# Performance work log

Hardware: AMD Instinct MI355X
Metric: run time of the kernel (lower is better)

Reference implementation:

```python
import jax, jax.numpy as jnp
import numpy as np

H = 128
NG, NS, NP = 50000, 20000, 30000
NUM_PC_FEATURES = 5
EPS = 1e-12


def seg_sum(x, idx, n):
    return jax.ops.segment_sum(x, idx, num_segments=n)


def seg_mean(x, idx, n):
    s = seg_sum(x, idx, n)
    cnt = seg_sum(jnp.ones((x.shape[0],), x.dtype), idx, n)
    return s / jnp.maximum(cnt, 1.0)[:, None]


def gcn_norm(row, col, n, add_self_loops):
    deg = seg_sum(jnp.ones(row.shape, jnp.float32), col, n)
    if add_self_loops:
        deg = deg + 1.0
    dinv = jnp.where(deg > 0, deg ** -0.5, 0.0)
    return dinv[row] * dinv[col], dinv


def tag_conv(x, row, col, n, Ws, b):
    # TAGConv: out = sum_k (A_hat^k x) W_k + b, symmetric norm, no self loops
    norm, _ = gcn_norm(row, col, n, False)
    out = x @ Ws[0]
    h = x
    for k in range(1, Ws.shape[0]):
        h = seg_sum(norm[:, None] * h[row], col, n)
        out = out + h @ Ws[k]
    return out + b


def rgcn_conv(x, row, col, etype, n, W, root, b):
    # RGCNConv: per-relation mean aggregation + root transform
    h = jnp.einsum('nc,rcd->rnd', x, W)  # [R, N, H]
    msg = h[etype, row]                  # [E, H]
    cnt = jnp.zeros((n, W.shape[0]), x.dtype).at[col, etype].add(1.0)
    w = 1.0 / jnp.maximum(cnt[col, etype], 1.0)
    return seg_sum(msg * w[:, None], col, n) + x @ root + b


def gcn_layer(x, row, col, n, W, b):
    # GCNConv: self loops + symmetric normalization
    xW = x @ W
    norm, dinv = gcn_norm(row, col, n, True)
    return seg_sum(norm[:, None] * xW[row], col, n) + (dinv ** 2)[:, None] * xW + b


def sage_conv(xs, xd, row, col, nd, lw, lb, rw):
    # SAGEConv with mean aggregation, root weight, L2 output normalization
    m = seg_mean(xs[row], col, nd)
    out = m @ lw + lb + xd @ rw
    nrm = jnp.maximum(jnp.linalg.norm(out, axis=-1, keepdims=True), EPS)
    return out / nrm


def setup_inputs() -> dict:
    key = jax.random.key(0)
    ks = iter(jax.random.split(key, 64))

    def nrm(shape):
        return jax.random.normal(next(ks), shape, jnp.float32) * 0.05

    def edges(ns, nd, e):
        return jnp.stack([jax.random.randint(next(ks), (e,), 0, ns, jnp.int32),
                          jax.random.randint(next(ks), (e,), 0, nd, jnp.int32)])

    return dict(
        game_x=nrm((NG, 7)),
        state_x=nrm((NS, 6)),
        pc_x=nrm((NP, NUM_PC_FEATURES)),
        edge_index_v_v=edges(NG, NG, 500000),
        edge_type_v_v=jax.random.randint(next(ks), (500000,), 0, 3, jnp.int32),
        edge_index_history_v_s=edges(NG, NS, 300000),
        edge_attr_history_v_s=nrm((300000, 2)),
        edge_index_in_v_s=edges(NG, NS, 300000),
        edge_index_s_s=edges(NS, NS, 200000),
        edge_index_pc_pc=edges(NP, NP, 300000),
        edge_index_pc_state=edges(NP, NS, 200000),
        edge_index_state_pc=edges(NS, NP, 100000),
        tag10_w=nrm((4, 7, H)), tag10_b=nrm((H,)),
        rgcn_w=nrm((3, H, H)), rgcn_root=nrm((H, H)), rgcn_b=nrm((H,)),
        gcn1_w=nrm((NUM_PC_FEATURES, H)), gcn1_b=nrm((H,)),
        gcn2_w=nrm((H, H)), gcn2_b=nrm((H,)),
        rg_key_w=nrm((6, H)), rg_key_b=nrm((H,)),
        rg_query_w=nrm((H, H)), rg_query_b=nrm((H,)),
        rg_value_w=nrm((H, H)), rg_value_b=nrm((H,)),
        rg_edge_w=nrm((2, H)), rg_skip_w=nrm((6, H)), rg_b=nrm((H,)),
        sage32_lw=nrm((H, H)), sage32_lb=nrm((H,)), sage32_rw=nrm((H, H)),
        sage4_lw=nrm((H, H)), sage4_lb=nrm((H,)), sage4_rw=nrm((H, H)),
        sage42_lw=nrm((H, H)), sage42_lb=nrm((H,)), sage42_rw=nrm((H, H)),
        pcs_lw=nrm((H, H)), pcs_lb=nrm((H,)), pcs_rw=nrm((H, H)),
        tag2_w=nrm((3, H, H)), tag2_b=nrm((H,)),
        sage5_lw=nrm((H, H)), sage5_lb=nrm((H,)), sage5_rw=nrm((H, H)),
        lin_w=nrm((H, 32)), lin_b=nrm((32,)),
        linl_w=nrm((32, 1)), linl_b=nrm((1,)),
    )


def reference(game_x, state_x, pc_x, edge_index_v_v, edge_type_v_v,
              edge_index_history_v_s, edge_attr_history_v_s, edge_index_in_v_s,
              edge_index_s_s, edge_index_pc_pc, edge_index_pc_state, edge_index_state_pc,
              tag10_w, tag10_b, rgcn_w, rgcn_root, rgcn_b,
              gcn1_w, gcn1_b, gcn2_w, gcn2_b,
              rg_key_w, rg_key_b, rg_query_w, rg_query_b, rg_value_w, rg_value_b,
              rg_edge_w, rg_skip_w, rg_b,
              sage32_lw, sage32_lb, sage32_rw,
              sage4_lw, sage4_lb, sage4_rw,
              sage42_lw, sage42_lb, sage42_rw,
              pcs_lw, pcs_lb, pcs_rw,
              tag2_w, tag2_b,
              sage5_lw, sage5_lb, sage5_rw,
              lin_w, lin_b, linl_w, linl_b):
    relu = jax.nn.relu
    rvv, cvv = edge_index_v_v[0], edge_index_v_v[1]
    g = relu(tag_conv(game_x, rvv, cvv, NG, tag10_w, tag10_b))
    g = relu(rgcn_conv(g, rvv, cvv, edge_type_v_v, NG, rgcn_w, rgcn_root, rgcn_b))
    rp, cp = edge_index_pc_pc[0], edge_index_pc_pc[1]
    p = relu(gcn_layer(pc_x, rp, cp, NP, gcn1_w, gcn1_b))
    p = relu(gcn_layer(p, rp, cp, NP, gcn2_w, gcn2_b))
    rh, ch = edge_index_history_v_s[0], edge_index_history_v_s[1]
    # ResGatedGraphConv((game, state), H, edge_dim=2)
    kk = state_x @ rg_key_w + rg_key_b
    q = g @ rg_query_w + rg_query_b
    v = g @ rg_value_w + rg_value_b
    e = edge_attr_history_v_s @ rg_edge_w
    eta = jax.nn.sigmoid(kk[ch] + q[rh] + e)
    s = relu(seg_sum(eta * v[rh], ch, NS) + state_x @ rg_skip_w + rg_b)
    s = relu(sage_conv(g, s, rh, ch, NS, sage32_lw, sage32_lb, sage32_rw))
    ri, ci = edge_index_in_v_s[0], edge_index_in_v_s[1]
    s = relu(sage_conv(g, s, ri, ci, NS, sage4_lw, sage4_lb, sage4_rw))
    s = relu(sage_conv(g, s, ri, ci, NS, sage42_lw, sage42_lb, sage42_rw))
    rps, cps = edge_index_pc_state[0], edge_index_pc_state[1]
    s = relu(sage_conv(p, s, rps, cps, NS, pcs_lw, pcs_lb, pcs_rw))
    rs, cs = edge_index_s_s[0], edge_index_s_s[1]
    s = relu(tag_conv(s, rs, cs, NS, tag2_w, tag2_b))
    s = relu(sage_conv(s, s, rs, cs, NS, sage5_lw, sage5_lb, sage5_rw))
    s = relu(s @ lin_w + lin_b)
    return jax.nn.log_softmax(s @ linl_w + linl_b, axis=0)
```

## Files before the change

### kernel.cpp

```cpp
#include <hip/hip_runtime.h>
#include <cstdint>

#define H 128
static const int NG = 50000, NS = 20000, NP = 30000;

#define TG_RELU 2
#define TG_NORM 4
#define TG_OUTBF16 8

#define CSR_CHUNK 8192

typedef __attribute__((ext_vector_type(8))) short bf16x8;
typedef __attribute__((ext_vector_type(4))) float f32x4;
typedef __attribute__((ext_vector_type(2))) float v2f;

static inline int nblk(long long n) { return (int)((n + 255) / 256); }

__device__ inline unsigned short f2b(float f) {
  unsigned int u = __float_as_uint(f);
  u += 0x7FFFu + ((u >> 16) & 1u);
  return (unsigned short)(u >> 16);
}
__device__ inline float b2f(unsigned short u) {
  return __uint_as_float(((unsigned int)u) << 16);
}
__device__ inline float2 bfp2(unsigned int u) {
  return make_float2(__uint_as_float(u << 16), __uint_as_float(u & 0xFFFF0000u));
}
__device__ inline unsigned int f2bfp(float x, float y) {
  return ((unsigned int)f2b(y) << 16) | (unsigned int)f2b(x);
}
__device__ inline float2 f8p2(unsigned short u) {
  v2f r = __builtin_amdgcn_cvt_pk_f32_fp8((int)(unsigned int)u, false);
  return make_float2(r.x, r.y);
}
__device__ inline unsigned char f2f8(float x) {
  int r = __builtin_amdgcn_cvt_pk_fp8_f32(x, 0.f, 0, false);
  return (unsigned char)(r & 0xFF);
}

struct Seg6 {
  const int* col[6];
  const int* row[6];
  const int* et0;
  int nodeoff[7];
  int edgeoff[7];
  int mode[6];
  float addself[6];
  int hasdinv[6];
};

__global__ __launch_bounds__(256) void k_hist(Seg6 sg, int EE, int* __restrict__ table) {
  __shared__ int h[512];
  int tid = threadIdx.x, blk = blockIdx.x;
  h[tid] = 0; h[tid + 256] = 0;
  __syncthreads();
  int e0 = blk * CSR_CHUNK, e1 = min(EE, e0 + CSR_CHUNK);
  for (int e = e0 + tid; e < e1; e += 256) {
    int gi = 0;
    while (e >= sg.edgeoff[gi + 1]) gi++;
    int le = e - sg.edgeoff[gi];
    int gn = sg.nodeoff[gi] + sg.col[gi][le];
    atomicAdd(&h[gn >> 9], 1);
  }
  __syncthreads();
  table[blk * 512 + tid] = h[tid];
  table[blk * 512 + tid + 256] = h[tid + 256];
}

__global__ void k_scanT(int* __restrict__ table, int nblkA, int* __restrict__ coarseOff) {
  int b = threadIdx.x;
  int s = 0;
  for (int k = 0; k < nblkA; k++) s += table[k * 512 + b];
  __shared__ int cs[512];
  cs[b] = s;
  __syncthreads();
  for (int off = 1; off < 512; off <<= 1) {
    int v = cs[b];
    int u = (b >= off) ? cs[b - off] : 0;
    __syncthreads();
    cs[b] = v + u;
    __syncthreads();
  }
  int excl = (b > 0) ? cs[b - 1] : 0;
  coarseOff[b] = excl;
  if (b == 511) coarseOff[512] = cs[511];
  int run = excl;
  for (int k = 0; k < nblkA; k++) {
    int t = table[k * 512 + b];
    table[k * 512 + b] = run;
    run += t;
  }
}

__global__ __launch_bounds__(256) void k_scatterA(Seg6 sg, int EE, const int* __restrict__ table,
                                                  uint2* __restrict__ tmp) {
  __shared__ int cur[512];
  int tid = threadIdx.x, blk = blockIdx.x;
  cur[tid] = table[blk * 512 + tid];
  cur[tid + 256] = table[blk * 512 + tid + 256];
  __syncthreads();
  int e0 = blk * CSR_CHUNK, e1 = min(EE, e0 + CSR_CHUNK);
  for (int e = e0 + tid; e < e1; e += 256) {
    int gi = 0;
    while (e >= sg.edgeoff[gi + 1]) gi++;
    int le = e - sg.edgeoff[gi];
    int gn = sg.nodeoff[gi] + sg.col[gi][le];
    int m = sg.mode[gi];
    int pay;
    if (m == 2) pay = le;
    else {
      pay = sg.row[gi][le];
      if (m == 1) pay |= sg.et0[le] << 16;
    }
    int pos = atomicAdd(&cur[gn >> 9], 1);
    tmp[pos] = make_uint2((unsigned)gn, (unsigned)pay);
  }
}

__global__ __launch_bounds__(256) void k_localCSR(const uint2* __restrict__ tmp,
                                                  const int* __restrict__ coarseOff,
                                                  Seg6 sg, int NN, int EE, int B,
                                                  int* __restrict__ rowptr,
                                                  int* __restrict__ eidx,
                                                  float* __restrict__ dinv) {
  int b = blockIdx.x, tid = threadIdx.x;
  int base = b * 512;
  int nNodes = min(512, NN - base);
  int beg = coarseOff[b], end = coarseOff[b + 1];
  __shared__ int cnt[512];
  __shared__ int off[512];
  __shared__ int ps[256];
  cnt[tid] = 0; cnt[tid + 256] = 0;
  __syncthreads();
  for (int j = beg + tid; j < end; j += 256)
    atomicAdd(&cnt[tmp[j].x - base], 1);
  __syncthreads();
  int a = cnt[2 * tid], bb = cnt[2 * tid + 1];
  ps[tid] = a + bb;
  __syncthreads();
  for (int o = 1; o < 256; o <<= 1) {
    int v = ps[tid];
    int u = (tid >= o) ? ps[tid - o] : 0;
    __syncthreads();
    ps[tid] = v + u;
    __syncthreads();
  }
  int excl = (tid > 0) ? ps[tid - 1] : 0;
  off[2 * tid] = excl;
  off[2 * tid + 1] = excl + a;
  __syncthreads();
  for (int i = tid; i < nNodes; i += 256) {
    int gid = base + i;
    rowptr[gid] = beg + off[i];
    int gi = 0;
    while (gid >= sg.nodeoff[gi + 1]) gi++;
    if (sg.hasdinv[gi]) {
      float d = (float)cnt[i] + sg.addself[gi];
      dinv[gid] = (d > 0.f) ? rsqrtf(d) : 0.f;
    }
  }
  if (b == B - 1 && tid == 0) rowptr[NN] = EE;
  __syncthreads();
  for (int j = beg + tid; j < end; j += 256) {
    uint2 p = tmp[j];
    int pos = beg + atomicAdd(&off[p.x - base], 1);
    eidx[pos] = (int)p.y;
  }
}

struct PackD { const float* src; int Ksrc; int Kdst; };
struct Pack17 { PackD d[17]; int koff[18]; };

__global__ void k_pack(Pack17 p, unsigned short* __restrict__ Wt, int totalRows) {
  int t = blockIdx.x * blockDim.x + threadIdx.x;
  if (t >= totalRows * 128) return;
  int gk = t >> 7, n = t & 127;
  int w = 0;
  while (gk >= p.koff[w + 1]) w++;
  int k = gk - p.koff[w];
  float v = (k < p.d[w].Ksrc) ? p.d[w].src[(size_t)k * 128 + n] : 0.f;
  Wt[(size_t)p.koff[w] * 128 + (size_t)n * p.d[w].Kdst + k] = f2b(v);
}

__global__ __launch_bounds__(256) void k_gmean(const unsigned short* __restrict__ src,
                                               const int* __restrict__ eidx,
                                               const int* __restrict__ rowptr,
                                               unsigned short* __restrict__ out, int N) {
  int c = blockIdx.x * 4 + (threadIdx.x >> 6);
  if (c >= N) return;
  int lane = threadIdx.x & 63;
  int beg = rowptr[c], end = rowptr[c + 1];
  float2 A0 = {0.f, 0.f}, A1 = {0.f, 0.f}, A2 = {0.f, 0.f}, A3 = {0.f, 0.f};
  int j = beg;
  for (; j + 4 <= end; j += 4) {
    int e0 = eidx[j], e1 = eidx[j + 1], e2 = eidx[j + 2], e3 = eidx[j + 3];
    float2 v0 = bfp2(*(const unsigned int*)(src + (size_t)e0 * H + lane * 2));
    float2 v1 = bfp2(*(const unsigned int*)(src + (size_t)e1 * H + lane * 2));
    float2 v2 = bfp2(*(const unsigned int*)(src + (size_t)e2 * H + lane * 2));
    float2 v3 = bfp2(*(const unsigned int*)(src + (size_t)e3 * H + lane * 2));
    A0.x += v0.x; A0.y += v0.y;
    A1.x += v1.x; A1.y += v1.y;
    A2.x += v2.x; A2.y += v2.y;
    A3.x += v3.x; A3.y += v3.y;
  }
  for (; j < end; j++) {
    float2 v = bfp2(*(const unsigned int*)(src + (size_t)eidx[j] * H + lane * 2));
    A0.x += v.x; A0.y += v.y;
  }
  int cnt = end - beg;
  float s = 1.f / (float)(cnt > 0 ? cnt : 1);
  float ox = (A0.x + A1.x + A2.x + A3.x) * s;
  float oy = (A0.y + A1.y + A2.y + A3.y) * s;
  *(unsigned int*)(out + (size_t)c * H + lane * 2) = f2bfp(ox, oy);
}

__global__ __launch_bounds__(256) void k_gmean_f8(const unsigned char* __restrict__ src,
                                                  const int* __restrict__ eidx,
                                                  const int* __restrict__ rowptr,
                                                  unsigned short* __restrict__ out, int N) {
  int c = blockIdx.x * 4 + (threadIdx.x >> 6);
  if (c >= N) return;
  int lane = threadIdx.x & 63;
  int beg = rowptr[c], end = rowptr[c + 1];
  float2 A0 = {0.f, 0.f}, A1 = {0.f, 0.f}, A2 = {0.f, 0.f}, A3 = {0.f, 0.f};
  int j = beg;
  for (; j + 4 <= end; j += 4) {
    int e0 = eidx[j], e1 = eidx[j + 1], e2 = eidx[j + 2], e3 = eidx[j + 3];
    float2 v0 = f8p2(*(const unsigned short*)(src + (size_t)e0 * H + lane * 2));
    float2 v1 = f8p2(*(const unsigned short*)(src + (size_t)e1 * H + lane * 2));
    float2 v2 = f8p2(*(const unsigned short*)(src + (size_t)e2 * H + lane * 2));
    float2 v3 = f8p2(*(const unsigned short*)(src + (size_t)e3 * H + lane * 2));
    A0.x += v0.x; A0.y += v0.y;
    A1.x += v1.x; A1.y += v1.y;
    A2.x += v2.x; A2.y += v2.y;
    A3.x += v3.x; A3.y += v3.y;
  }
  for (; j < end; j++) {
    float2 v = f8p2(*(const unsigned short*)(src + (size_t)eidx[j] * H + lane * 2));
    A0.x += v.x; A0.y += v.y;
  }
  int cnt = end - beg;
  float s = 1.f / (float)(cnt > 0 ? cnt : 1);
  float ox = (A0.x + A1.x + A2.x + A3.x) * s;
  float oy = (A0.y + A1.y + A2.y + A3.y) * s;
  *(unsigned int*)(out + (size_t)c * H + lane * 2) = f2bfp(ox, oy);
}

__global__ __launch_bounds__(256) void k_grel3(const unsigned char* __restrict__ src,
                                               const int* __restrict__ eidx,
                                               const int* __restrict__ rowptr,
                                               unsigned short* __restrict__ G3, int N) {
  int c = blockIdx.x * 4 + (threadIdx.x >> 6);
  if (c >= N) return;
  int lane = threadIdx.x & 63;
  int beg = rowptr[c], end = rowptr[c + 1];
  float2 a0 = {0.f, 0.f}, a1 = {0.f, 0.f}, a2 = {0.f, 0.f};
  int c0 = 0, c1 = 0, c2 = 0;
  int j = beg;
  for (; j + 4 <= end; j += 4) {
    int p0 = eidx[j], p1 = eidx[j + 1], p2 = eidx[j + 2], p3 = eidx[j + 3];
    float2 w0 = f8p2(*(const unsigned short*)(src + (size_t)(p0 & 0xFFFF) * H + lane * 2));
    float2 w1 = f8p2(*(const unsigned short*)(src + (size_t)(p1 & 0xFFFF) * H + lane * 2));
    float2 w2 = f8p2(*(const unsigned short*)(src + (size_t)(p2 & 0xFFFF) * H + lane * 2));
    float2 w3 = f8p2(*(const unsigned short*)(src + (size_t)(p3 & 0xFFFF) * H + lane * 2));
    int r0 = p0 >> 16, r1 = p1 >> 16, r2 = p2 >> 16, r3 = p3 >> 16;
    if (r0 == 0) { a0.x += w0.x; a0.y += w0.y; c0++; }
    else if (r0 == 1) { a1.x += w0.x; a1.y += w0.y; c1++; }
    else { a2.x += w0.x; a2.y += w0.y; c2++; }
    if (r1 == 0) { a0.x += w1.x; a0.y += w1.y; c0++; }
    else if (r1 == 1) { a1.x += w1.x; a1.y += w1.y; c1++; }
    else { a2.x += w1.x; a2.y += w1.y; c2++; }
    if (r2 == 0) { a0.x += w2.x; a0.y += w2.y; c0++; }
    else if (r2 == 1) { a1.x += w2.x; a1.y += w2.y; c1++; }
    else { a2.x += w2.x; a2.y += w2.y; c2++; }
    if (r3 == 0) { a0.x += w3.x; a0.y += w3.y; c0++; }
    else if (r3 == 1) { a1.x += w3.x; a1.y += w3.y; c1++; }
    else { a2.x += w3.x; a2.y += w3.y; c2++; }
  }
  for (; j < end; j++) {
    int pk = eidx[j];
    int rel = pk >> 16;
    float2 v = f8p2(*(const unsigned short*)(src + (size_t)(pk & 0xFFFF) * H + lane * 2));
    if (rel == 0) { a0.x += v.x; a0.y += v.y; c0++; }
    else if (rel == 1) { a1.x += v.x; a1.y += v.y; c1++; }
    else { a2.x += v.x; a2.y += v.y; c2++; }
  }
  float s0 = 1.f / (float)(c0 > 0 ? c0 : 1);
  float s1 = 1.f / (float)(c1 > 0 ? c1 : 1);
  float s2 = 1.f / (float)(c2 > 0 ? c2 : 1);
  size_t base = (size_t)c * 384 + lane * 2;
  *(unsigned int*)(G3 + base) = f2bfp(a0.x * s0, a0.y * s0);
  *(unsigned int*)(G3 + base + 128) = f2bfp(a1.x * s1, a1.y * s1);
  *(unsigned int*)(G3 + base + 256) = f2bfp(a2.x * s2, a2.y * s2);
}

__global__ __launch_bounds__(256) void k_gnorm(const unsigned short* __restrict__ src,
                                               long ldS, int offS,
                                               const int* __restrict__ eidx,
                                               const int* __restrict__ rowptr,
                                               const float* __restrict__ dinv,
                                               const unsigned short* __restrict__ selfX,
                                               const float* __restrict__ bias,
                                               unsigned short* __restrict__ out,
                                               long ldD, int offD, int relu, int N) {
  int c = blockIdx.x * 4 + (threadIdx.x >> 6);
  if (c >= N) return;
  int lane = threadIdx.x & 63;
  int beg = rowptr[c], end = rowptr[c + 1];
  float2 A0 = {0.f, 0.f}, A1 = {0.f, 0.f}, A2 = {0.f, 0.f}, A3 = {0.f, 0.f};
  int j = beg;
  for (; j + 4 <= end; j += 4) {
    int e0 = eidx[j], e1 = eidx[j + 1], e2 = eidx[j + 2], e3 = eidx[j + 3];
    float w0 = dinv[e0], w1 = dinv[e1], w2 = dinv[e2], w3 = dinv[e3];
    float2 v0 = bfp2(*(const unsigned int*)(src + (size_t)e0 * ldS + offS + lane * 2));
    float2 v1 = bfp2(*(const unsigned int*)(src + (size_t)e1 * ldS + offS + lane * 2));
    float2 v2 = bfp2(*(const unsigned int*)(src + (size_t)e2 * ldS + offS + lane * 2));
    float2 v3 = bfp2(*(const unsigned int*)(src + (size_t)e3 * ldS + offS + lane * 2));
    A0.x = fmaf(w0, v0.x, A0.x); A0.y = fmaf(w0, v0.y, A0.y);
    A1.x = fmaf(w1, v1.x, A1.x); A1.y = fmaf(w1, v1.y, A1.y);
    A2.x = fmaf(w2, v2.x, A2.x); A2.y = fmaf(w2, v2.y, A2.y);
    A3.x = fmaf(w3, v3.x, A3.x); A3.y = fmaf(w3, v3.y, A3.y);
  }
  for (; j < end; j++) {
    int e = eidx[j];
    float w = dinv[e];
    float2 v = bfp2(*(const unsigned int*)(src + (size_t)e * ldS + offS + lane * 2));
    A0.x = fmaf(w, v.x, A0.x); A0.y = fmaf(w, v.y, A0.y);
  }
  float dc = dinv[c];
  float ox = (A0.x + A1.x + A2.x + A3.x) * dc;
  float oy = (A0.y + A1.y + A2.y + A3.y) * dc;
  if (selfX) {
    float2 sv = bfp2(*(const unsigned int*)(selfX + (size_t)c * H + lane * 2));
    ox += dc * dc * sv.x;
    oy += dc * dc * sv.y;
  }
  if (bias) {
    float2 bv = *(const float2*)(bias + lane * 2);
    ox += bv.x; oy += bv.y;
  }
  if (relu) { ox = fmaxf(ox, 0.f); oy = fmaxf(oy, 0.f); }
  *(unsigned int*)(out + (size_t)c * ldD + offD + lane * 2) = f2bfp(ox, oy);
}

__global__ __launch_bounds__(256) void k_resgated_mean(const unsigned short* __restrict__ kk,
                                                       const unsigned char* __restrict__ q,
                                                       const unsigned char* __restrict__ v,
                                                       const unsigned char* __restrict__ g,
                                                       const float* __restrict__ ea,
                                                       const float* __restrict__ We,
                                                       const int* __restrict__ rh,
                                                       const int* __restrict__ eidx,
                                                       const int* __restrict__ rowptr,
                                                       const float* __restrict__ sx,
                                                       const float* __restrict__ Wsk,
                                                       const float* __restrict__ rgb,
                                                       unsigned short* __restrict__ outS,
                                                       unsigned short* __restrict__ outM, int N) {
  int c = blockIdx.x * 4 + (threadIdx.x >> 6);
  if (c >= N) return;
  int lane = threadIdx.x & 63;
  int d0 = lane * 2;
  int beg = rowptr[c], end = rowptr[c + 1];
  float2 kload = bfp2(*(const unsigned int*)(kk + (size_t)c * H + d0));
  float2 we0 = make_float2(We[d0], We[d0 + 1]);
  float2 we1 = make_float2(We[H + d0], We[H + d0 + 1]);
  float2 accS = {0.f, 0.f}, accM = {0.f, 0.f};
  int j = beg;
  for (; j + 4 <= end; j += 4) {
    int e0 = eidx[j], e1 = eidx[j + 1], e2 = eidx[j + 2], e3 = eidx[j + 3];
    int r0 = rh[e0], r1 = rh[e1], r2 = rh[e2], r3 = rh[e3];
    float2 ea0 = *(const float2*)(ea + 2 * e0);
    float2 ea1 = *(const float2*)(ea + 2 * e1);
    float2 ea2 = *(const float2*)(ea + 2 * e2);
    float2 ea3 = *(const float2*)(ea + 2 * e3);
    unsigned short uq0 = *(const unsigned short*)(q + (size_t)r0 * H + d0);
    unsigned short uv0 = *(const unsigned short*)(v + (size_t)r0 * H + d0);
    unsigned short ug0 = *(const unsigned short*)(g + (size_t)r0 * H + d0);
    unsigned short uq1 = *(const unsigned short*)(q + (size_t)r1 * H + d0);
    unsigned short uv1 = *(const unsigned short*)(v + (size_t)r1 * H + d0);
    unsigned short ug1 = *(const unsigned short*)(g + (size_t)r1 * H + d0);
    unsigned short uq2 = *(const unsigned short*)(q + (size_t)r2 * H + d0);
    unsigned short uv2 = *(const unsigned short*)(v + (size_t)r2 * H + d0);
    unsigned short ug2 = *(const unsigned short*)(g + (size_t)r2 * H + d0);
    unsigned short uq3 = *(const unsigned short*)(q + (size_t)r3 * H + d0);
    unsigned short uv3 = *(const unsigned short*)(v + (size_t)r3 * H + d0);
    unsigned short ug3 = *(const unsigned short*)(g + (size_t)r3 * H + d0);
#define RG_STEP(UQ, UV, UG, EA)                                            \
    {                                                                      \
      float2 qv = f8p2(UQ);                                                \
      float2 vv = f8p2(UV);                                                \
      float2 gv = f8p2(UG);                                                \
      float x0 = kload.x + qv.x + (EA).x * we0.x + (EA).y * we1.x;         \
      float x1 = kload.y + qv.y + (EA).x * we0.y + (EA).y * we1.y;         \
      float eta0 = 1.f / (1.f + __expf(-x0));                              \
      float eta1 = 1.f / (1.f + __expf(-x1));                              \
      accS.x = fmaf(eta0, vv.x, accS.x);                                   \
      accS.y = fmaf(eta1, vv.y, accS.y);                                   \
      accM.x += gv.x; accM.y += gv.y;                                      \
    }
    RG_STEP(uq0, uv0, ug0, ea0)
    RG_STEP(uq1, uv1, ug1, ea1)
    RG_STEP(uq2, uv2, ug2, ea2)
    RG_STEP(uq3, uv3, ug3, ea3)
  }
  for (; j < end; j++) {
    int e = eidx[j];
    int r = rh[e];
    float2 eav = *(const float2*)(ea + 2 * e);
    unsigned short uq = *(const unsigned short*)(q + (size_t)r * H + d0);
    unsigned short uv = *(const unsigned short*)(v + (size_t)r * H + d0);
    unsigned short ug = *(const unsigned short*)(g + (size_t)r * H + d0);
    RG_STEP(uq, uv, ug, eav)
  }
#undef RG_STEP
  float sk0 = rgb[d0], sk1 = rgb[d0 + 1];
#pragma unroll
  for (int f = 0; f < 6; f++) {
    float xf = sx[c * 6 + f];
    sk0 = fmaf(xf, Wsk[f * H + d0], sk0);
    sk1 = fmaf(xf, Wsk[f * H + d0 + 1], sk1);
  }
  *(unsigned int*)(outS + (size_t)c * H + d0) =
      f2bfp(fmaxf(accS.x + sk0, 0.f), fmaxf(accS.y + sk1, 0.f));
  int cnt = end - beg;
  float s = 1.f / (float)(cnt > 0 ? cnt : 1);
  *(unsigned int*)(outM + (size_t)c * H + d0) = f2bfp(accM.x * s, accM.y * s);
}

__global__ __launch_bounds__(256) void k_gnorm7w(const unsigned short* __restrict__ src,
                                                 int ldS, int offS,
                                                 const int* __restrict__ eidx,
                                                 const int* __restrict__ rowptr,
                                                 const float* __restrict__ dinv,
                                                 unsigned short* __restrict__ dst,
                                                 int ldD, int offD, int N) {
  int c = blockIdx.x * 4 + (threadIdx.x >> 6);
  if (c >= N) return;
  int lane = threadIdx.x & 63;
  int eg = lane >> 3, f = lane & 7;
  int beg = rowptr[c], end = rowptr[c + 1];
  float acc = 0.f;
  for (int j = beg + eg; j < end; j += 8) {
    int r = eidx[j] & 0xFFFF;
    float w = dinv[r];
    float val = (f < 7) ? b2f(src[(size_t)r * ldS + offS + f]) : 0.f;
    acc = fmaf(w, val, acc);
  }
  acc += __shfl_xor(acc, 8);
  acc += __shfl_xor(acc, 16);
  acc += __shfl_xor(acc, 32);
  if (eg == 0 && f < 7)
    dst[(size_t)c * ldD + offD + f] = f2b(acc * dinv[c]);
}

__global__ void k_copy7b(const float* __restrict__ src, unsigned short* __restrict__ dst, int n) {
  long long t = (long long)blockIdx.x * blockDim.x + threadIdx.x;
  int i = (int)(t >> 3), f = (int)(t & 7);
  if (i < n && f < 7) dst[(size_t)i * 32 + f] = f2b(src[(size_t)i * 7 + f]);
}

__global__ void k_gemm128b(const float* __restrict__ X, const float* __restrict__ W,
                           const float* __restrict__ b, unsigned short* __restrict__ out,
                           int M, int K) {
  long long t = (long long)blockIdx.x * blockDim.x + threadIdx.x;
  if (t >= (long long)M * H) return;
  int i = (int)(t >> 7), h = (int)(t & 127);
  float acc = b ? b[h] : 0.f;
  const float* x = X + (long long)i * K;
  for (int k = 0; k < K; k++) acc = fmaf(x[k], W[k * H + h], acc);
  out[t] = f2b(acc);
}

__global__ __launch_bounds__(256) void k_mgemm(const unsigned short* __restrict__ X1, int ldX1, int K1,
                                               const unsigned short* __restrict__ W1t,
                                               const unsigned short* __restrict__ X2, int ldX2, int K2,
                                               const unsigned short* __restrict__ W2t,
                                               const float* __restrict__ bias,
                                               void* __restrict__ Cv, long ldC,
                                               int M, int flags,
                                               unsigned char* __restrict__ C8) {
  __shared__ unsigned short Als[64 * 40];
  __shared__ unsigned short Bls[128 * 40];
  __shared__ float rs[2][64];
  int tid = threadIdx.x;
  int lane = tid & 63, wv = tid >> 6;
  int m = lane & 15, q = lane >> 4;
  int rbase = (wv & 1) * 32;
  int cbase = (wv >> 1) * 64;
  int blockRow = blockIdx.x * 64;
  int sr = tid >> 2, skc = (tid & 3) * 8;
  f32x4 acc[2][4];
#pragma unroll
  for (int a = 0; a < 2; a++)
#pragma unroll
    for (int b = 0; b < 4; b++) acc[a][b] = (f32x4){0.f, 0.f, 0.f, 0.f};

  int Ktot = K1 + K2;
  for (int k0 = 0; k0 < Ktot; k0 += 32) {
    const unsigned short* Xb;
    const unsigned short* Wt_;
    int kr, ldx, Kw;
    if (k0 < K1) { Xb = X1; Wt_ = W1t; kr = k0; ldx = ldX1; Kw = K1; }
    else { Xb = X2; Wt_ = W2t; kr = k0 - K1; ldx = ldX2; Kw = K2; }
    __syncthreads();
    {
      int gr = blockRow + sr;
      bf16x8 xv = (bf16x8){0, 0, 0, 0, 0, 0, 0, 0};
      if (gr < M) xv = *(const bf16x8*)(Xb + (size_t)gr * ldx + kr + skc);
      *(bf16x8*)&Als[sr * 40 + skc] = xv;
    }
#pragma unroll
    for (int it = 0; it < 2; it++) {
      int fid = it * 256 + tid;
      int n = fid >> 2, kc = (fid & 3) * 8;
      *(bf16x8*)&Bls[n * 40 + kc] = *(const bf16x8*)(Wt_ + (size_t)n * Kw + kr + kc);
    }
    __syncthreads();
    bf16x8 a0 = *(const bf16x8*)&Als[(rbase + m) * 40 + q * 8];
    bf16x8 a1 = *(const bf16x8*)&Als[(rbase + 16 + m) * 40 + q * 8];
    bf16x8 b0 = *(const bf16x8*)&Bls[(cbase + m) * 40 + q * 8];
    bf16x8 b1 = *(const bf16x8*)&Bls[(cbase + 16 + m) * 40 + q * 8];
    bf16x8 b2 = *(const bf16x8*)&Bls[(cbase + 32 + m) * 40 + q * 8];
    bf16x8 b3 = *(const bf16x8*)&Bls[(cbase + 48 + m) * 40 + q * 8];
    acc[0][0] = __builtin_amdgcn_mfma_f32_16x16x32_bf16(a0, b0, acc[0][0], 0, 0, 0);
    acc[0][1] = __builtin_amdgcn_mfma_f32_16x16x32_bf16(a0, b1, acc[0][1], 0, 0, 0);
    acc[0][2] = __builtin_amdgcn_mfma_f32_16x16x32_bf16(a0, b2, acc[0][2], 0, 0, 0);
    acc[0][3] = __builtin_amdgcn_mfma_f32_16x16x32_bf16(a0, b3, acc[0][3], 0, 0, 0);
    acc[1][0] = __builtin_amdgcn_mfma_f32_16x16x32_bf16(a1, b0, acc[1][0], 0, 0, 0);
    acc[1][1] = __builtin_amdgcn_mfma_f32_16x16x32_bf16(a1, b1, acc[1][1], 0, 0, 0);
    acc[1][2] = __builtin_amdgcn_mfma_f32_16x16x32_bf16(a1, b2, acc[1][2], 0, 0, 0);
    acc[1][3] = __builtin_amdgcn_mfma_f32_16x16x32_bf16(a1, b3, acc[1][3], 0, 0, 0);
  }
  float ov[2][4][4];
  float bcol[4] = {0.f, 0.f, 0.f, 0.f};
  if (bias) {
#pragma unroll
    for (int j = 0; j < 4; j++) bcol[j] = bias[cbase + j * 16 + m];
  }
#pragma unroll
  for (int a = 0; a < 2; a++)
#pragma unroll
    for (int j = 0; j < 4; j++)
#pragma unroll
      for (int i = 0; i < 4; i++) ov[a][j][i] = acc[a][j][i] + bcol[j];

  if (flags & TG_NORM) {
#pragma unroll
    for (int a = 0; a < 2; a++)
#pragma unroll
      for (int i = 0; i < 4; i++) {
        float p = 0.f;
#pragma unroll
        for (int j = 0; j < 4; j++) p = fmaf(ov[a][j][i], ov[a][j][i], p);
        p += __shfl_xor(p, 1);
        p += __shfl_xor(p, 2);
        p += __shfl_xor(p, 4);
        p += __shfl_xor(p, 8);
        if (m == 0) rs[wv >> 1][rbase + a * 16 + q * 4 + i] = p;
      }
    __syncthreads();
#pragma unroll
    for (int a = 0; a < 2; a++)
#pragma unroll
      for (int i = 0; i < 4; i++) {
        int ridx = rbase + a * 16 + q * 4 + i;
        float s = rs[0][ridx] + rs[1][ridx];
        float f = 1.f / fmaxf(sqrtf(s), 1e-12f);
#pragma unroll
        for (int j = 0; j < 4; j++) ov[a][j][i] = fmaxf(ov[a][j][i] * f, 0.f);
      }
  } else if (flags & TG_RELU) {
#pragma unroll
    for (int a = 0; a < 2; a++)
#pragma unroll
      for (int j = 0; j < 4; j++)
#pragma unroll
        for (int i = 0; i < 4; i++) ov[a][j][i] = fmaxf(ov[a][j][i], 0.f);
  }
  if (flags & TG_OUTBF16) {
    unsigned short* C = (unsigned short*)Cv;
#pragma unroll
    for (int a = 0; a < 2; a++)
#pragma unroll
      for (int i = 0; i < 4; i++) {
        int row = blockRow + rbase + a * 16 + q * 4 + i;
        if (row < M) {
#pragma unroll
          for (int j = 0; j < 4; j++)
            C[(size_t)row * ldC + cbase + j * 16 + m] = f2b(ov[a][j][i]);
        }
      }
  } else {
    float* C = (float*)Cv;
#pragma unroll
    for (int a = 0; a < 2; a++)
#pragma unroll
      for (int i = 0; i < 4; i++) {
        int row = blockRow + rbase + a * 16 + q * 4 + i;
        if (row < M) {
#pragma unroll
          for (int j = 0; j < 4; j++)
            C[(size_t)row * ldC + cbase + j * 16 + m] = ov[a][j][i];
        }
      }
  }
  if (C8) {
#pragma unroll
    for (int a = 0; a < 2; a++)
#pragma unroll
      for (int i = 0; i < 4; i++) {
        int row = blockRow + rbase + a * 16 + q * 4 + i;
        if (row < M) {
#pragma unroll
          for (int j = 0; j < 4; j++)
            C8[(size_t)row * ldC + cbase + j * 16 + m] = f2f8(ov[a][j][i]);
        }
      }
  }
}

static inline int mgb(int M) { return (M + 63) / 64; }

__global__ __launch_bounds__(256) void k_head(const float* __restrict__ X,
                                              const float* __restrict__ lw,
                                              const float* __restrict__ lb,
                                              const float* __restrict__ lwl,
                                              const float* __restrict__ lbl,
                                              float* __restrict__ z, int M) {
  __shared__ float Wl[128 * 32];
  __shared__ float Xs[8][128];
  int tid = threadIdx.x;
  for (int i = tid * 4; i < 4096; i += 1024) *(float4*)&Wl[i] = *(const float4*)&lw[i];
  int rowBase = blockIdx.x * 8;
  {
    int idx = tid * 4;
    int xr = idx >> 7, xc = idx & 127;
    int grow = rowBase + xr;
    float4 v = make_float4(0.f, 0.f, 0.f, 0.f);
    if (grow < M) v = *(const float4*)(X + (size_t)grow * H + xc);
    *(float4*)&Xs[xr][xc] = v;
  }
  __syncthreads();
  int r = tid >> 5, o = tid & 31;
  float acc = lb[o];
  for (int k = 0; k < 128; k++) acc = fmaf(Xs[r][k], Wl[k * 32 + o], acc);
  acc = fmaxf(acc, 0.f) * lwl[o];
  for (int s = 16; s > 0; s >>= 1) acc += __shfl_down(acc, s, 32);
  int grow = rowBase + r;
  if (o == 0 && grow < M) z[grow] = acc + lbl[0];
}

__global__ void k_logsoftmax(const float* __restrict__ z, float* __restrict__ out, int n) {
  __shared__ float red[256];
  int tid = threadIdx.x;
  float m = -1e30f;
  for (int i = tid; i < n; i += 256) m = fmaxf(m, z[i]);
  red[tid] = m;
  __syncthreads();
  for (int s = 128; s > 0; s >>= 1) {
    if (tid < s) red[tid] = fmaxf(red[tid], red[tid + s]);
    __syncthreads();
  }
  float mx = red[0];
  __syncthreads();
  float sum = 0.f;
  for (int i = tid; i < n; i += 256) sum += __expf(z[i] - mx);
  red[tid] = sum;
  __syncthreads();
  for (int s = 128; s > 0; s >>= 1) {
    if (tid < s) red[tid] += red[tid + s];
    __syncthreads();
  }
  float lse = mx + logf(red[0]);
  for (int i = tid; i < n; i += 256) out[i] = z[i] - lse;
}

extern "C" void kernel_launch(void* const* d_in, const int* in_sizes, int n_in,
                              void* d_out, int out_size, void* d_ws, size_t ws_size,
                              hipStream_t stream) {
  const float* game_x = (const float*)d_in[0];
  const float* state_x = (const float*)d_in[1];
  const float* pc_x = (const float*)d_in[2];
  const int* ei_vv = (const int*)d_in[3];
  const int* et_vv = (const int*)d_in[4];
  const int* ei_hist = (const int*)d_in[5];
  const float* ea_hist = (const float*)d_in[6];
  const int* ei_in = (const int*)d_in[7];
  const int* ei_ss = (const int*)d_in[8];
  const int* ei_pp = (const int*)d_in[9];
  const int* ei_ps = (const int*)d_in[10];
  const float* tag10_w = (const float*)d_in[12];
  const float* tag10_b = (const float*)d_in[13];
  const float* rgcn_w = (const float*)d_in[14];
  const float* rgcn_root = (const float*)d_in[15];
  const float* rgcn_b = (const float*)d_in[16];
  const float* gcn1_w = (const float*)d_in[17];
  const float* gcn1_b = (const float*)d_in[18];
  const float* gcn2_w = (const float*)d_in[19];
  const float* gcn2_b = (const float*)d_in[20];
  const float* rg_key_w = (const float*)d_in[21];
  const float* rg_key_b = (const float*)d_in[22];
  const float* rg_query_w = (const float*)d_in[23];
  const float* rg_query_b = (const float*)d_in[24];
  const float* rg_value_w = (const float*)d_in[25];
  const float* rg_value_b = (const float*)d_in[26];
  const float* rg_edge_w = (const float*)d_in[27];
  const float* rg_skip_w = (const float*)d_in[28];
  const float* rg_b = (const float*)d_in[29];
  const float* sage32_lw = (const float*)d_in[30];
  const float* sage32_lb = (const float*)d_in[31];
  const float* sage32_rw = (const float*)d_in[32];
  const float* sage4_lw = (const float*)d_in[33];
  const float* sage4_lb = (const float*)d_in[34];
  const float* sage4_rw = (const float*)d_in[35];
  const float* sage42_lw = (const float*)d_in[36];
  const float* sage42_lb = (const float*)d_in[37];
  const float* sage42_rw = (const float*)d_in[38];
  const float* pcs_lw = (const float*)d_in[39];
  const float* pcs_lb = (const float*)d_in[40];
  const float* pcs_rw = (const float*)d_in[41];
  const float* tag2_w = (const float*)d_in[42];
  const float* tag2_b = (const float*)d_in[43];
  const float* sage5_lw = (const float*)d_in[44];
  const float* sage5_lb = (const float*)d_in[45];
  const float* sage5_rw = (const float*)d_in[46];
  const float* lin_w = (const float*)d_in[47];
  const float* lin_b = (const float*)d_in[48];
  const float* linl_w = (const float*)d_in[49];
  const float* linl_b = (const float*)d_in[50];

  const int Evv = in_sizes[3] / 2, Eh = in_sizes[5] / 2, Ein = in_sizes[7] / 2,
            Ess = in_sizes[8] / 2, Epp = in_sizes[9] / 2, Eps = in_sizes[10] / 2;
  const int EE = Evv + Epp + Eh + Ein + Eps + Ess;
  const int NN = NG + NP + 4 * NS;

  char* base = (char*)d_ws;
  const size_t B_NGH = (size_t)NG * H * 2;
  const size_t B_NPH = (size_t)NP * H * 2;
  const size_t B_NSH = (size_t)NS * H * 2;
  unsigned short* g_tag_b = (unsigned short*)base;
  unsigned short* g_b = (unsigned short*)(base + B_NGH);
  char* C0 = base + 2 * B_NGH;
  uint2* tmp_pairs = (uint2*)C0;
  unsigned short* P_tag10_b = (unsigned short*)C0;
  unsigned short* G3_b = (unsigned short*)C0;
  unsigned short* xW_b = (unsigned short*)C0;
  unsigned short* p1b_b = (unsigned short*)(C0 + B_NPH);
  unsigned short* p2b_b = (unsigned short*)(C0 + 2 * B_NPH);
  unsigned short* v_b = (unsigned short*)C0;
  unsigned short* q_b = g_tag_b;
  unsigned short* P_tag2_b = (unsigned short*)C0;
  char* S0 = base + 2 * B_NGH + 46000000;
  unsigned short* S_a_b = (unsigned short*)S0;
  unsigned short* S_b_b = (unsigned short*)(S0 + B_NSH);
  unsigned short* m_buf_b = (unsigned short*)(S0 + 2 * B_NSH);
  unsigned short* kk_b = (unsigned short*)(S0 + 3 * B_NSH);
  float* Sfin = (float*)(S0 + 4 * B_NSH);
  unsigned short* Wt = (unsigned short*)(S0 + 4 * B_NSH + (size_t)NS * H * 4);
  int* ip = (int*)(S0 + 4 * B_NSH + (size_t)NS * H * 4 + 700000);
  int* rp_all = ip; ip += NN + 1;
  int* eidx_all = ip; ip += EE;
  int* table = ip; ip += 512 * 240;
  int* coarseOff = ip; ip += 520;
  float* fp = (float*)ip;
  float* dinv_all = fp; fp += NN;
  float* z = fp; fp += NS;
  unsigned char* g_tag_8 = (unsigned char*)(z + NS);
  unsigned char* g_8 = g_tag_8 + (size_t)NG * H;
  unsigned char* q_8 = g_8 + (size_t)NG * H;
  unsigned char* v_8 = q_8 + (size_t)NG * H;

  Seg6 sg;
  sg.col[0] = ei_vv + Evv;  sg.row[0] = ei_vv;
  sg.col[1] = ei_pp + Epp;  sg.row[1] = ei_pp;
  sg.col[2] = ei_hist + Eh; sg.row[2] = ei_hist;
  sg.col[3] = ei_in + Ein;  sg.row[3] = ei_in;
  sg.col[4] = ei_ps + Eps;  sg.row[4] = ei_ps;
  sg.col[5] = ei_ss + Ess;  sg.row[5] = ei_ss;
  sg.et0 = et_vv;
  int no[7] = {0, NG, NG + NP, NG + NP + NS, NG + NP + 2 * NS, NG + NP + 3 * NS, NN};
  int eo[7] = {0, Evv, Evv + Epp, Evv + Epp + Eh, Evv + Epp + Eh + Ein,
               Evv + Epp + Eh + Ein + Eps, EE};
  for (int i = 0; i < 7; i++) { sg.nodeoff[i] = no[i]; sg.edgeoff[i] = eo[i]; }
  int md[6] = {1, 0, 2, 0, 0, 0};
  float as[6] = {0.f, 1.f, 0.f, 0.f, 0.f, 0.f};
  int hd[6] = {1, 1, 0, 0, 0, 1};
  for (int i = 0; i < 6; i++) { sg.mode[i] = md[i]; sg.addself[i] = as[i]; sg.hasdinv[i] = hd[i]; }

  const int* rp_vv = rp_all + no[0];
  const int* rp_pp = rp_all + no[1];
  const int* rp_hh = rp_all + no[2];
  const int* rp_in = rp_all + no[3];
  const int* rp_ps = rp_all + no[4];
  const int* rp_ss = rp_all + no[5];
  const float* dinvG = dinv_all + no[0];
  const float* dinvP = dinv_all + no[1];
  const float* dinvS = dinv_all + no[5];
  const int* rh = ei_hist;

  Pack17 pk;
  const float* wsrc[17] = {tag10_w, rgcn_w, rgcn_root, gcn2_w, rg_query_w, rg_value_w,
                           sage32_lw, sage32_rw, sage4_lw, sage4_rw, sage42_lw, sage42_rw,
                           pcs_lw, pcs_rw, tag2_w, sage5_lw, sage5_rw};
  int ksrc[17] = {28, 384, 128, 128, 128, 128, 128, 128, 128, 128, 128, 128, 128, 128, 384, 128, 128};
  int kdst[17] = {32, 384, 128, 128, 128, 128, 128, 128, 128, 128, 128, 128, 128, 128, 384, 128, 128};
  int run = 0;
  for (int i = 0; i < 17; i++) {
    pk.d[i].src = wsrc[i]; pk.d[i].Ksrc = ksrc[i]; pk.d[i].Kdst = kdst[i];
    pk.koff[i] = run; run += kdst[i];
  }
  pk.koff[17] = run;
  unsigned short* WT[17];
  for (int i = 0; i < 17; i++) WT[i] = Wt + (size_t)pk.koff[i] * 128;
  k_pack<<<nblk((long long)run * 128), 256, 0, stream>>>(pk, Wt, run);

  int nblkA = (EE + CSR_CHUNK - 1) / CSR_CHUNK;
  int B = (NN + 511) / 512;
  k_hist<<<nblkA, 256, 0, stream>>>(sg, EE, table);
  k_scanT<<<1, 512, 0, stream>>>(table, nblkA, coarseOff);
  k_scatterA<<<nblkA, 256, 0, stream>>>(sg, EE, table, tmp_pairs);
  k_localCSR<<<B, 256, 0, stream>>>(tmp_pairs, coarseOff, sg, NN, EE, B,
                                    rp_all, eidx_all, dinv_all);

  hipMemsetAsync(P_tag10_b, 0, (size_t)NG * 32 * 2, stream);
  k_copy7b<<<nblk((long long)NG * 8), 256, 0, stream>>>(game_x, P_tag10_b, NG);
  k_gnorm7w<<<(NG + 3) / 4, 256, 0, stream>>>(P_tag10_b, 32, 0, eidx_all, rp_vv, dinvG,
                                              P_tag10_b, 32, 7, NG);
  k_gnorm7w<<<(NG + 3) / 4, 256, 0, stream>>>(P_tag10_b, 32, 7, eidx_all, rp_vv, dinvG,
                                              P_tag10_b, 32, 14, NG);
  k_gnorm7w<<<(NG + 3) / 4, 256, 0, stream>>>(P_tag10_b, 32, 14, eidx_all, rp_vv, dinvG,
                                              P_tag10_b, 32, 21, NG);
  k_mgemm<<<mgb(NG), 256, 0, stream>>>(P_tag10_b, 32, 32, WT[0], nullptr, 0, 0, nullptr,
                                       tag10_b, g_tag_b, H, NG, TG_RELU | TG_OUTBF16, g_tag_8);

  k_grel3<<<(NG + 3) / 4, 256, 0, stream>>>(g_tag_8, eidx_all, rp_vv, G3_b, NG);
  k_mgemm<<<mgb(NG), 256, 0, stream>>>(G3_b, 384, 384, WT[1], g_tag_b, H, H, WT[2],
                                       rgcn_b, g_b, H, NG, TG_RELU | TG_OUTBF16, g_8);

  k_gemm128b<<<nblk((long long)NP * H), 256, 0, stream>>>(pc_x, gcn1_w, nullptr, xW_b, NP, 5);
  k_gnorm<<<(NP + 3) / 4, 256, 0, stream>>>(xW_b, H, 0, eidx_all, rp_pp, dinvP, xW_b, gcn1_b,
                                            p1b_b, H, 0, 1, NP);
  k_mgemm<<<mgb(NP), 256, 0, stream>>>(p1b_b, H, H, WT[3], nullptr, 0, 0, nullptr,
                                       nullptr, xW_b, H, NP, TG_OUTBF16, nullptr);
  k_gnorm<<<(NP + 3) / 4, 256, 0, stream>>>(xW_b, H, 0, eidx_all, rp_pp, dinvP, xW_b, gcn2_b,
                                            p2b_b, H, 0, 1, NP);

  k_gemm128b<<<nblk((long long)NS * H), 256, 0, stream>>>(state_x, rg_key_w, rg_key_b, kk_b, NS, 6);
  k_mgemm<<<mgb(NG), 256, 0, stream>>>(g_b, H, H, WT[4], nullptr, 0, 0, nullptr,
                                       rg_query_b, q_b, H, NG, TG_OUTBF16, q_8);
  k_mgemm<<<mgb(NG), 256, 0, stream>>>(g_b, H, H, WT[5], nullptr, 0, 0, nullptr,
                                       rg_value_b, v_b, H, NG, TG_OUTBF16, v_8);
  k_resgated_mean<<<(NS + 3) / 4, 256, 0, stream>>>(kk_b, q_8, v_8, g_8, ea_hist, rg_edge_w, rh,
                                                    eidx_all, rp_hh, state_x, rg_skip_w, rg_b,
                                                    S_a_b, m_buf_b, NS);

  k_mgemm<<<mgb(NS), 256, 0, stream>>>(m_buf_b, H, H, WT[6], S_a_b, H, H, WT[7],
                                       sage32_lb, S_b_b, H, NS, TG_NORM | TG_OUTBF16, nullptr);

  k_gmean_f8<<<(NS + 3) / 4, 256, 0, stream>>>(g_8, eidx_all, rp_in, m_buf_b, NS);
  k_mgemm<<<mgb(NS), 256, 0, stream>>>(m_buf_b, H, H, WT[8], S_b_b, H, H, WT[9],
                                       sage4_lb, S_a_b, H, NS, TG_NORM | TG_OUTBF16, nullptr);
  k_mgemm<<<mgb(NS), 256, 0, stream>>>(m_buf_b, H, H, WT[10], S_a_b, H, H, WT[11],
                                       sage42_lb, S_b_b, H, NS, TG_NORM | TG_OUTBF16, nullptr);

  k_gmean<<<(NS + 3) / 4, 256, 0, stream>>>(p2b_b, eidx_all, rp_ps, m_buf_b, NS);
  k_mgemm<<<mgb(NS), 256, 0, stream>>>(m_buf_b, H, H, WT[12], S_b_b, H, H, WT[13],
                                       pcs_lb, P_tag2_b, 384, NS, TG_NORM | TG_OUTBF16, nullptr);

  k_gnorm<<<(NS + 3) / 4, 256, 0, stream>>>(P_tag2_b, 384, 0, eidx_all, rp_ss, dinvS, nullptr,
                                            nullptr, P_tag2_b, 384, 128, 0, NS);
  k_gnorm<<<(NS + 3) / 4, 256, 0, stream>>>(P_tag2_b, 384, 128, eidx_all, rp_ss, dinvS, nullptr,
                                            nullptr, P_tag2_b, 384, 256, 0, NS);
  k_mgemm<<<mgb(NS), 256, 0, stream>>>(P_tag2_b, 384, 384, WT[14], nullptr, 0, 0, nullptr,
                                       tag2_b, S_b_b, H, NS, TG_RELU | TG_OUTBF16, nullptr);

  k_gmean<<<(NS + 3) / 4, 256, 0, stream>>>(S_b_b, eidx_all, rp_ss, m_buf_b, NS);
  k_mgemm<<<mgb(NS), 256, 0, stream>>>(m_buf_b, H, H, WT[15], S_b_b, H, H, WT[16],
                                       sage5_lb, Sfin, H, NS, TG_NORM, nullptr);

  k_head<<<(NS + 7) / 8, 256, 0, stream>>>(Sfin, lin_w, lin_b, linl_w, linl_b, z, NS);
  k_logsoftmax<<<1, 256, 0, stream>>>(z, (float*)d_out, NS);
}
```

Measured before the change: 753.7 us.

## Parallelize CSR coarse-bucket scan across blocks with three-phase scan

The single-block column scan over the histogram table, where each thread looped serially over every chunk row twice, is replaced by three kernels. The first does a per-bucket parallel scan across chunks with 512 blocks. The second scans the 512 bucket totals, and the third adds the bucket offsets back into the table. This removes a latency-bound serial loop from the CSR build at the cost of two extra kernel launches. It also assumes there are at most 256 chunks.

```diff
diff --git a/kernel.cpp b/kernel.cpp
--- a/kernel.cpp
+++ b/kernel.cpp
@@ -68,12 +68,30 @@
   table[blk * 512 + tid + 256] = h[tid + 256];
 }
 
-__global__ void k_scanT(int* __restrict__ table, int nblkA, int* __restrict__ coarseOff) {
+__global__ __launch_bounds__(256) void k_scanT1(int* __restrict__ table, int nblkA,
+                                                int* __restrict__ colsum) {
+  __shared__ int s[256];
+  int b = blockIdx.x;
+  int t = threadIdx.x;
+  int v = (t < nblkA) ? table[t * 512 + b] : 0;
+  s[t] = v;
+  __syncthreads();
+  for (int off = 1; off < 256; off <<= 1) {
+    int x = s[t];
+    int u = (t >= off) ? s[t - off] : 0;
+    __syncthreads();
+    s[t] = x + u;
+    __syncthreads();
+  }
+  int excl = (t > 0) ? s[t - 1] : 0;
+  if (t < nblkA) table[t * 512 + b] = excl;
+  if (t == 255) colsum[b] = s[255];
+}
+
+__global__ void k_scanT2(const int* __restrict__ colsum, int* __restrict__ coarseOff) {
+  __shared__ int cs[512];
   int b = threadIdx.x;
-  int s = 0;
-  for (int k = 0; k < nblkA; k++) s += table[k * 512 + b];
-  __shared__ int cs[512];
-  cs[b] = s;
+  cs[b] = colsum[b];
   __syncthreads();
   for (int off = 1; off < 512; off <<= 1) {
     int v = cs[b];
@@ -82,15 +100,13 @@
     cs[b] = v + u;
     __syncthreads();
   }
-  int excl = (b > 0) ? cs[b - 1] : 0;
-  coarseOff[b] = excl;
+  coarseOff[b] = (b > 0) ? cs[b - 1] : 0;
   if (b == 511) coarseOff[512] = cs[511];
-  int run = excl;
-  for (int k = 0; k < nblkA; k++) {
-    int t = table[k * 512 + b];
-    table[k * 512 + b] = run;
-    run += t;
-  }
+}
+
+__global__ void k_scanT3(int* __restrict__ table, const int* __restrict__ coarseOff, int n) {
+  int i = blockIdx.x * blockDim.x + threadIdx.x;
+  if (i < n) table[i] += coarseOff[i & 511];
 }
 
 __global__ __launch_bounds__(256) void k_scatterA(Seg6 sg, int EE, const int* __restrict__ table,
@@ -764,6 +780,7 @@
   int* eidx_all = ip; ip += EE;
   int* table = ip; ip += 512 * 240;
   int* coarseOff = ip; ip += 520;
+  int* colsum = ip; ip += 512;
   float* fp = (float*)ip;
   float* dinv_all = fp; fp += NN;
   float* z = fp; fp += NS;
@@ -819,7 +836,9 @@
   int nblkA = (EE + CSR_CHUNK - 1) / CSR_CHUNK;
   int B = (NN + 511) / 512;
   k_hist<<<nblkA, 256, 0, stream>>>(sg, EE, table);
-  k_scanT<<<1, 512, 0, stream>>>(table, nblkA, coarseOff);
+  k_scanT1<<<512, 256, 0, stream>>>(table, nblkA, colsum);
+  k_scanT2<<<1, 512, 0, stream>>>(colsum, coarseOff);
+  k_scanT3<<<nblk((long long)nblkA * 512), 256, 0, stream>>>(table, coarseOff, nblkA * 512);
   k_scatterA<<<nblkA, 256, 0, stream>>>(sg, EE, table, tmp_pairs);
   k_localCSR<<<B, 256, 0, stream>>>(tmp_pairs, coarseOff, sg, NN, EE, B,
                                     rp_all, eidx_all, dinv_all);
```

Result: faster. 707.6 us (-6.1%).
